# Performance work log

Measured on AMD Instinct MI355X. Metric: run time of the kernel, lower is better.

The kernel has to match this reference:

```python
import jax, jax.numpy as jnp
import numpy as np

B, T, H, STEPS = 8192, 128, 128, 30
BN_EPS = 1e-5


def gru_cell(x, h, w_ih, w_hh, b_ih, b_hh):
    # PyTorch GRU gate math: gates ordered (r, z, n)
    gi = x @ w_ih.T + b_ih            # [B, 3H]
    gh = h @ w_hh.T + b_hh            # [B, 3H]
    ir, iz, inn = jnp.split(gi, 3, axis=-1)
    hr, hz, hn = jnp.split(gh, 3, axis=-1)
    r = jax.nn.sigmoid(ir + hr)
    z = jax.nn.sigmoid(iz + hz)
    n = jnp.tanh(inn + r * hn)
    return (1.0 - z) * n + z * h


def setup_inputs() -> dict:
    key = jax.random.key(0)
    ks = jax.random.split(key, 10)
    s = lambda k, shape: jax.random.normal(k, shape, jnp.float32) * 0.05
    z = lambda *shape: jnp.zeros(shape, jnp.float32)
    return {
        "past": jax.random.normal(ks[0], (B, 6, T), jnp.float32),
        "conv_w": s(ks[1], (H, 6, 3)),
        "conv_b": z(H),
        "bn_gamma": jnp.ones((1,), jnp.float32),
        "bn_beta": z(1),
        "bn_mean": z(1),
        "bn_var": jnp.ones((1,), jnp.float32),
        "enc_wih": s(ks[2], (3 * H, H)),
        "enc_whh": s(ks[3], (3 * H, H)),
        "enc_bih": z(3 * H),
        "enc_bhh": z(3 * H),
        "dec_wih": s(ks[4], (3 * H, H)),
        "dec_whh": s(ks[5], (3 * H, H)),
        "dec_bih": z(3 * H),
        "dec_bhh": z(3 * H),
        "fc1_w": s(ks[6], (256, H)),
        "fc1_b": z(256),
        "fc2_w": s(ks[7], (64, 256)),
        "fc2_b": z(64),
        "fc3_w": s(ks[8], (6, 64)),
        "fc3_b": z(6),
    }


def reference(past, conv_w, conv_b, bn_gamma, bn_beta, bn_mean, bn_var,
              enc_wih, enc_whh, enc_bih, enc_bhh,
              dec_wih, dec_whh, dec_bih, dec_bhh,
              fc1_w, fc1_b, fc2_w, fc2_b, fc3_w, fc3_b):
    b = past.shape[0]
    # Conv1d(6 -> 128, k=3, pad=1) + ReLU
    y = jax.lax.conv_general_dilated(
        past, conv_w, window_strides=(1,), padding=[(1, 1)],
        dimension_numbers=("NCH", "OIH", "NCH"))
    y = jax.nn.relu(y + conv_b[None, :, None])
    # BatchNorm2d(1) in eval mode: single-channel affine normalization over whole tensor
    y = bn_gamma[0] * (y - bn_mean[0]) * jax.lax.rsqrt(bn_var[0] + BN_EPS) + bn_beta[0]
    # encoder GRU over time: [B,128,T] -> [T,B,128]
    xs = jnp.transpose(y, (2, 0, 1))
    h0 = jnp.zeros((b, H), y.dtype)

    def enc_step(h, x):
        return gru_cell(x, h, enc_wih, enc_whh, enc_bih, enc_bhh), None

    state_past, _ = jax.lax.scan(enc_step, h0, xs)  # [B,128]

    def mlp(h):
        a = jax.nn.relu(h @ fc1_w.T + fc1_b)
        a = a @ fc2_w.T + fc2_b   # no activation between fc2 and fc3 (matches Sequential)
        return a @ fc3_w.T + fc3_b

    # decoder input is state_past at step 0, zeros afterwards
    dec_inputs = jnp.concatenate(
        [state_past[None], jnp.zeros((STEPS - 1, b, H), y.dtype)], axis=0)
    present0 = past[:, :, -1]  # [B,6]

    def dec_step(carry, x):
        h, present = carry
        h = gru_cell(x, h, dec_wih, dec_whh, dec_bih, dec_bhh)
        present = present + mlp(h)
        return (h, present), present

    _, preds = jax.lax.scan(dec_step, (jnp.zeros((b, H), y.dtype), present0), dec_inputs)
    # preds: [30,B,6] -> [B,6,30] (matches prediction.permute(0,2,1))
    return jnp.transpose(preds, (1, 2, 0))
```

## Files before the change

### kernel.cpp

```cpp
#include <hip/hip_runtime.h>

#define DI __device__ __forceinline__

typedef __attribute__((ext_vector_type(8))) short short8;
typedef __attribute__((ext_vector_type(4))) float f32x4;

constexpr int THREADS = 512;
constexpr int ROWS    = 32;
constexpr int NBLK    = 8192 / ROWS;
constexpr int PITCH   = 272;
constexpr int PITCH2  = 528;
constexpr int SPITCH  = 256;

constexpr float L2E  = 1.4426950408889634f;
constexpr float L2E2 = 2.8853900817779268f;

constexpr int O_STAGE = 0;
constexpr int O_PATCH = 98304;
constexpr int O_XALL  = 108544;
constexpr int O_H     = 143360;
constexpr int HBUF    = 8704;
constexpr int O_FC3W  = 160768;
constexpr int LDS_TOTAL = 162304;
constexpr int O_A1D   = 98304;
constexpr int O_W32   = 115200;
constexpr int O_B32   = 123648;
constexpr int O_A1D2  = 123680;

DI unsigned cvtpk2(float lo, float hi){
  unsigned r;
  asm("v_cvt_pk_bf16_f32 %0, %1, %2" : "=v"(r) : "v"(lo), "v"(hi));
  return r;
}
DI unsigned short f2bf(float f){ return (unsigned short)cvtpk2(f, f); }
DI float u2f_lo(unsigned u){ union { unsigned u; float f; } v; v.u = u << 16;        return v.f; }
DI float u2f_hi(unsigned u){ union { unsigned u; float f; } v; v.u = u & 0xffff0000u; return v.f; }
DI float exp2n(float x){ float r; asm("v_exp_f32 %0, -%1" : "=v"(r) : "v"(x)); return r; }
DI float sigm2(float s){ return __builtin_amdgcn_rcpf(1.f + exp2n(s)); }
DI float tanh2(float s){ return 2.f * __builtin_amdgcn_rcpf(1.f + exp2n(s)) - 1.f; }
DI f32x4 mfma16(short8 a, short8 b, f32x4 c){
  return __builtin_amdgcn_mfma_f32_16x16x32_bf16(a, b, c, 0, 0, 0);
}
DI uint2 pack4(f32x4 v){
  return make_uint2(cvtpk2(v[0], v[1]), cvtpk2(v[2], v[3]));
}
DI f32x4 unpack4(uint2 u){
  return (f32x4){u2f_lo(u.x), u2f_hi(u.x), u2f_lo(u.y), u2f_hi(u.y)};
}

DI void stage_k128(char* dst, const float* __restrict__ src, int nrows, int tid,
                   float sA, float sB){
  const int total = nrows * 32;
  for (int i = tid; i < total; i += THREADS){
    float4 v = ((const float4*)src)[i];
    int e = i << 2;
    int n = e >> 7, k = e & 127;
    float sc = (n < 256) ? sA : sB;
    *(uint2*)(dst + n * SPITCH + k * 2) =
        make_uint2(cvtpk2(v.x * sc, v.y * sc), cvtpk2(v.z * sc, v.w * sc));
  }
}

__global__ void __launch_bounds__(THREADS, 1)
gru_fused(const float* __restrict__ past,
          const float* __restrict__ conv_w, const float* __restrict__ conv_b,
          const float* __restrict__ bn_gamma, const float* __restrict__ bn_beta,
          const float* __restrict__ bn_mean, const float* __restrict__ bn_var,
          const float* __restrict__ enc_wih, const float* __restrict__ enc_whh,
          const float* __restrict__ enc_bih, const float* __restrict__ enc_bhh,
          const float* __restrict__ dec_wih, const float* __restrict__ dec_whh,
          const float* __restrict__ dec_bih, const float* __restrict__ dec_bhh,
          const float* __restrict__ fc1_w, const float* __restrict__ fc1_b,
          const float* __restrict__ fc2_w, const float* __restrict__ fc2_b,
          const float* __restrict__ fc3_w, const float* __restrict__ fc3_b,
          float* __restrict__ out)
{
  extern __shared__ char smem[];
  const int tid  = threadIdx.x;
  const int lane = tid & 63, w = tid >> 6;
  const int l15  = lane & 15, quad = lane >> 4;
  const int b0   = blockIdx.x * ROWS;
  const int col  = w * 16 + l15;

  const float br_e  = (enc_bih[col]       + enc_bhh[col])       * L2E;
  const float bz_e  = (enc_bih[128 + col] + enc_bhh[128 + col]) * L2E;
  const float bin_e = enc_bih[256 + col] * L2E2;
  const float bhn_e = enc_bhh[256 + col] * L2E2;
  const float br_d  = (dec_bih[col]       + dec_bhh[col])       * L2E;
  const float bz_d  = (dec_bih[128 + col] + dec_bhh[128 + col]) * L2E;
  const float bin_d = dec_bih[256 + col] * L2E2;
  const float bhn_d = dec_bhh[256 + col] * L2E2;
  const float cb_t  = conv_b[col];
  const float s_bn  = bn_gamma[0] * rsqrtf(bn_var[0] + 1e-5f);
  const float o_bn  = bn_beta[0] - bn_mean[0] * s_bn;
  const float fb1a  = fc1_b[w * 32 + l15];
  const float fb1b  = fc1_b[w * 32 + 16 + l15];

  for (int i = tid; i < 2*HBUF/4; i += THREADS) ((unsigned*)(smem + O_H))[i] = 0u;

  short8 wf[3][4], wh[3][4];
  stage_k128(smem + O_STAGE, enc_wih, 384, tid, L2E, L2E2);
  __syncthreads();
  #pragma unroll
  for (int g = 0; g < 3; ++g)
    #pragma unroll
    for (int kt = 0; kt < 4; ++kt)
      wf[g][kt] = *(const short8*)(smem + O_STAGE + (g*128 + col)*SPITCH + kt*64 + quad*16);
  __syncthreads();
  stage_k128(smem + O_STAGE, enc_whh, 384, tid, L2E, L2E2);
  __syncthreads();
  #pragma unroll
  for (int g = 0; g < 3; ++g)
    #pragma unroll
    for (int kt = 0; kt < 4; ++kt)
      wh[g][kt] = *(const short8*)(smem + O_STAGE + (g*128 + col)*SPITCH + kt*64 + quad*16);
  __syncthreads();

  for (int i = tid; i < 2560; i += THREADS) ((unsigned*)(smem + O_STAGE))[i] = 0u;
  __syncthreads();
  for (int i = tid; i < 2304; i += THREADS){
    int oc = i / 18, kk = i - oc * 18;
    *(unsigned short*)(smem + O_STAGE + oc*80 + kk*2) = f2bf(conv_w[i]);
  }
  __syncthreads();
  const short8 cwf = *(const short8*)(smem + O_STAGE + col*80 + quad*16);
  __syncthreads();

  for (int i = tid; i < 12672; i += THREADS) ((unsigned*)(smem + O_STAGE))[i] = 0u;
  __syncthreads();
  for (int i4 = tid; i4 < 6144; i4 += THREADS){
    int m = i4 / 192, rem = i4 - m*192, c = rem >> 5, t4 = (rem & 31) << 2;
    float4 v = *(const float4*)(past + (size_t)(b0 + m)*768 + c*128 + t4);
    unsigned short* dst = (unsigned short*)(smem + O_STAGE + ((m*6 + c)*132 + t4 + 1)*2);
    dst[0] = f2bf(v.x); dst[1] = f2bf(v.y); dst[2] = f2bf(v.z); dst[3] = f2bf(v.w);
  }
  for (int i = tid; i < 384; i += THREADS) ((float*)(smem + O_FC3W))[i] = fc3_w[i];
  __syncthreads();

  const int e0 = tid;
  const int m0 = e0 / 18, r0 = e0 - m0*18, c0 = r0 / 3, k0 = r0 - c0*3;
  const int e1 = tid + 512;
  const int m1 = e1 / 18, r1 = e1 - m1*18, c1 = r1 / 3, k1 = r1 - c1*3;

  auto patch_entry = [&](int t0, int m, int r18, int c, int k){
    int base = (m*6 + c)*132 + t0 + k;
    const unsigned* pl = (const unsigned*)(smem + O_STAGE);
    unsigned w0 = pl[base >> 1], w1 = pl[(base >> 1) + 1], w2 = pl[(base >> 1) + 2];
    int sh = (base & 1) * 16;
    unsigned long long lo = (unsigned long long)w0 | ((unsigned long long)w1 << 32);
    unsigned long long hi = (unsigned long long)w1 | ((unsigned long long)w2 << 32);
    unsigned a01 = (unsigned)(lo >> sh);
    unsigned a23 = (unsigned)(hi >> sh);
    char* pb = smem + O_PATCH + m*80 + r18*2;
    *(unsigned short*)(pb)          = (unsigned short)(a01 & 0xffff);
    *(unsigned short*)(pb + 2560)   = (unsigned short)(a01 >> 16);
    *(unsigned short*)(pb + 5120)   = (unsigned short)(a23 & 0xffff);
    *(unsigned short*)(pb + 7680)   = (unsigned short)(a23 >> 16);
  };
  auto patchA1 = [&](int t0){
    patch_entry(t0, m0, r0, c0, k0);
    if (e1 < 576) patch_entry(t0, m1, r1, c1, k1);
  };

  uint2 gi_pk[4][2][3];
  float hreg[8];
  #pragma unroll
  for (int i = 0; i < 8; ++i) hreg[i] = 0.f;

  auto conv_block = [&](){
    #pragma unroll
    for (int mt8 = 0; mt8 < 8; ++mt8){
      short8 pa = *(const short8*)(smem + O_PATCH + (mt8*16 + l15)*80 + quad*16);
      f32x4 cc = (f32x4){0.f,0.f,0.f,0.f};
      cc = mfma16(pa, cwf, cc);
      #pragma unroll
      for (int r = 0; r < 4; ++r){
        int mrow = mt8*16 + quad*4 + r;
        float vx = s_bn * fmaxf(cc[r] + cb_t, 0.f) + o_bn;
        *(unsigned short*)(smem + O_XALL + mrow*PITCH + col*2) = f2bf(vx);
      }
    }
  };
  auto gi_unit = [&](int tc, int mt){
    short8 a[4];
    #pragma unroll
    for (int kt = 0; kt < 4; ++kt)
      a[kt] = *(const short8*)(smem + O_XALL + ((tc*2 + mt)*16 + l15)*PITCH + kt*64 + quad*16);
    f32x4 g0 = (f32x4){0.f,0.f,0.f,0.f}, g1 = g0, g2 = g0;
    #pragma unroll
    for (int kt = 0; kt < 4; ++kt){
      g0 = mfma16(a[kt], wf[0][kt], g0);
      g1 = mfma16(a[kt], wf[1][kt], g1);
      g2 = mfma16(a[kt], wf[2][kt], g2);
    }
    gi_pk[tc][mt][0] = pack4(g0);
    gi_pk[tc][mt][1] = pack4(g1);
    gi_pk[tc][mt][2] = pack4(g2);
  };
  auto step_body = [&](int t, int tc){
    const char* hr = smem + O_H + (t & 1) * HBUF;
    char*       hw = smem + O_H + ((t + 1) & 1) * HBUF;
    f32x4 accr[2], accz[2], accn2[2], gin[2];
    #pragma unroll
    for (int mt = 0; mt < 2; ++mt){
      accr[mt]  = unpack4(gi_pk[tc][mt][0]);
      accz[mt]  = unpack4(gi_pk[tc][mt][1]);
      gin[mt]   = unpack4(gi_pk[tc][mt][2]);
      accn2[mt] = (f32x4){0.f,0.f,0.f,0.f};
    }
    short8 ha[2][4];
    #pragma unroll
    for (int mt = 0; mt < 2; ++mt)
      #pragma unroll
      for (int kt = 0; kt < 4; ++kt)
        ha[mt][kt] = *(const short8*)(hr + (mt*16 + l15)*PITCH + kt*64 + quad*16);
    #pragma unroll
    for (int mt = 0; mt < 2; ++mt)
      #pragma unroll
      for (int kt = 0; kt < 4; ++kt){
        accr[mt]  = mfma16(ha[mt][kt], wh[0][kt], accr[mt]);
        accz[mt]  = mfma16(ha[mt][kt], wh[1][kt], accz[mt]);
        accn2[mt] = mfma16(ha[mt][kt], wh[2][kt], accn2[mt]);
      }
    #pragma unroll
    for (int mt = 0; mt < 2; ++mt)
      #pragma unroll
      for (int r = 0; r < 4; ++r){
        float rg = sigm2(accr[mt][r] + br_e);
        float zg = sigm2(accz[mt][r] + bz_e);
        float ng = tanh2(gin[mt][r] + bin_e + rg*(accn2[mt][r] + bhn_e));
        hreg[mt*4 + r] = ng + zg*(hreg[mt*4 + r] - ng);
      }
    #pragma unroll
    for (int mt = 0; mt < 2; ++mt)
      #pragma unroll
      for (int r = 0; r < 4; ++r)
        *(unsigned short*)(hw + (mt*16 + quad*4 + r)*PITCH + col*2) = f2bf(hreg[mt*4 + r]);
  };

  patchA1(0);
  __syncthreads();
  conv_block();
  __syncthreads();
  #pragma unroll
  for (int tc = 0; tc < 4; ++tc){ gi_unit(tc, 0); gi_unit(tc, 1); }
  patchA1(4);
  __syncthreads();

  for (int c = 0; c < 32; ++c){
    const int t0 = c * 4;
    const bool prod = (c < 31);
    step_body(t0 + 0, 0);
    if (prod) conv_block();
    __syncthreads();
    step_body(t0 + 1, 1);
    if (prod){ gi_unit(0,0); gi_unit(0,1); gi_unit(1,0); }
    __syncthreads();
    step_body(t0 + 2, 2);
    if (prod){ gi_unit(1,1); gi_unit(2,0); gi_unit(2,1); }
    __syncthreads();
    step_body(t0 + 3, 3);
    if (prod){ gi_unit(3,0); gi_unit(3,1); if (c < 30) patchA1(t0 + 8); }
    __syncthreads();
  }

  stage_k128(smem + O_STAGE, dec_wih, 384, tid, L2E, L2E2);
  __syncthreads();
  #pragma unroll
  for (int g = 0; g < 3; ++g)
    #pragma unroll
    for (int kt = 0; kt < 4; ++kt)
      wf[g][kt] = *(const short8*)(smem + O_STAGE + (g*128 + col)*SPITCH + kt*64 + quad*16);
  f32x4 gi0r[2], gi0z[2], gi0n[2];
  {
    short8 hea[2][4];
    #pragma unroll
    for (int mt = 0; mt < 2; ++mt)
      #pragma unroll
      for (int kt = 0; kt < 4; ++kt)
        hea[mt][kt] = *(const short8*)(smem + O_H + (mt*16 + l15)*PITCH + kt*64 + quad*16);
    #pragma unroll
    for (int mt = 0; mt < 2; ++mt){
      gi0r[mt] = (f32x4){0.f,0.f,0.f,0.f}; gi0z[mt] = gi0r[mt]; gi0n[mt] = gi0r[mt];
      #pragma unroll
      for (int kt = 0; kt < 4; ++kt){
        gi0r[mt] = mfma16(hea[mt][kt], wf[0][kt], gi0r[mt]);
        gi0z[mt] = mfma16(hea[mt][kt], wf[1][kt], gi0z[mt]);
        gi0n[mt] = mfma16(hea[mt][kt], wf[2][kt], gi0n[mt]);
      }
    }
  }
  __syncthreads();
  stage_k128(smem + O_STAGE, dec_whh, 384, tid, L2E, L2E2);
  __syncthreads();
  #pragma unroll
  for (int g = 0; g < 3; ++g)
    #pragma unroll
    for (int kt = 0; kt < 4; ++kt)
      wh[g][kt] = *(const short8*)(smem + O_STAGE + (g*128 + col)*SPITCH + kt*64 + quad*16);
  __syncthreads();
  short8 f1f[2][4];
  stage_k128(smem + O_STAGE, fc1_w, 256, tid, 1.f, 1.f);
  __syncthreads();
  #pragma unroll
  for (int j = 0; j < 2; ++j)
    #pragma unroll
    for (int kt = 0; kt < 4; ++kt)
      f1f[j][kt] = *(const short8*)(smem + O_STAGE + (w*32 + j*16 + l15)*SPITCH + kt*64 + quad*16);
  __syncthreads();

  for (int i = tid; i < 2112; i += THREADS) ((unsigned*)(smem + O_W32))[i] = 0u;
  __syncthreads();
  {
    const int kk = tid & 255, wn = (tid >> 8) * 3;
    const float* f3p = (const float*)(smem + O_FC3W);
    float o0 = 0.f, o1 = 0.f, o2 = 0.f;
    for (int j = 0; j < 64; ++j){
      float cv = fc2_w[j*256 + kk];
      o0 += f3p[(wn+0)*64 + j] * cv;
      o1 += f3p[(wn+1)*64 + j] * cv;
      o2 += f3p[(wn+2)*64 + j] * cv;
    }
    *(unsigned short*)(smem + O_W32 + (wn+0)*PITCH2 + kk*2) = f2bf(o0);
    *(unsigned short*)(smem + O_W32 + (wn+1)*PITCH2 + kk*2) = f2bf(o1);
    *(unsigned short*)(smem + O_W32 + (wn+2)*PITCH2 + kk*2) = f2bf(o2);
    if (tid < 6){
      float ob = fc3_b[tid];
      for (int j = 0; j < 64; ++j) ob += f3p[tid*64 + j] * fc2_b[j];
      ((float*)(smem + O_B32))[tid] = ob;
    }
  }
  for (int i = tid; i < HBUF/4; i += THREADS) ((unsigned*)(smem + O_H + HBUF))[i] = 0u;
  #pragma unroll
  for (int i = 0; i < 8; ++i) hreg[i] = 0.f;
  __syncthreads();
  float pres[4] = {0.f, 0.f, 0.f, 0.f};
  float b32v = 0.f;
  if (w < 2 && l15 < 6){
    b32v = ((const float*)(smem + O_B32))[l15];
    #pragma unroll
    for (int r = 0; r < 4; ++r)
      pres[r] = past[(size_t)(b0 + w*16 + quad*4 + r)*768 + l15*128 + 127];
  }

  auto fc23 = [&](int sIdx){
    const char* a1b = smem + ((sIdx & 1) ? O_A1D2 : O_A1D);
    f32x4 acc = (f32x4){0.f,0.f,0.f,0.f};
    #pragma unroll
    for (int kt = 0; kt < 8; ++kt){
      short8 a   = *(const short8*)(a1b + (w*16 + l15)*PITCH2 + kt*64 + quad*16);
      short8 bfr = *(const short8*)(smem + O_W32 + l15*PITCH2 + kt*64 + quad*16);
      acc = mfma16(a, bfr, acc);
    }
    if (l15 < 6){
      #pragma unroll
      for (int r = 0; r < 4; ++r){
        pres[r] += acc[r] + b32v;
        out[(size_t)(b0 + w*16 + quad*4 + r)*180 + l15*30 + sIdx] = pres[r];
      }
    }
  };

  for (int s = 0; s < 30; ++s){
    const char* hr = smem + O_H + (1 - (s & 1)) * HBUF;
    char*       hw = smem + O_H + (s & 1) * HBUF;
    f32x4 accr[2], accz[2], accn2[2], gin[2];
    #pragma unroll
    for (int mt = 0; mt < 2; ++mt){
      if (s == 0){ accr[mt] = gi0r[mt]; accz[mt] = gi0z[mt]; gin[mt] = gi0n[mt]; }
      else       { accr[mt] = (f32x4){0.f,0.f,0.f,0.f}; accz[mt] = accr[mt]; gin[mt] = accr[mt]; }
      accn2[mt] = (f32x4){0.f,0.f,0.f,0.f};
    }
    {
      short8 ha[2][4];
      #pragma unroll
      for (int mt = 0; mt < 2; ++mt)
        #pragma unroll
        for (int kt = 0; kt < 4; ++kt)
          ha[mt][kt] = *(const short8*)(hr + (mt*16 + l15)*PITCH + kt*64 + quad*16);
      #pragma unroll
      for (int mt = 0; mt < 2; ++mt)
        #pragma unroll
        for (int kt = 0; kt < 4; ++kt){
          accr[mt]  = mfma16(ha[mt][kt], wh[0][kt], accr[mt]);
          accz[mt]  = mfma16(ha[mt][kt], wh[1][kt], accz[mt]);
          accn2[mt] = mfma16(ha[mt][kt], wh[2][kt], accn2[mt]);
        }
    }
    #pragma unroll
    for (int mt = 0; mt < 2; ++mt)
      #pragma unroll
      for (int r = 0; r < 4; ++r){
        float rg = sigm2(accr[mt][r] + br_d);
        float zg = sigm2(accz[mt][r] + bz_d);
        float ng = tanh2(gin[mt][r] + bin_d + rg*(accn2[mt][r] + bhn_d));
        hreg[mt*4 + r] = ng + zg*(hreg[mt*4 + r] - ng);
      }
    #pragma unroll
    for (int mt = 0; mt < 2; ++mt)
      #pragma unroll
      for (int r = 0; r < 4; ++r)
        *(unsigned short*)(hw + (mt*16 + quad*4 + r)*PITCH + col*2) = f2bf(hreg[mt*4 + r]);
    __syncthreads();

    if (s > 0 && w < 2) fc23(s - 1);

    {
      char* a1w = smem + ((s & 1) ? O_A1D2 : O_A1D);
      short8 hf[2][4];
      #pragma unroll
      for (int mt = 0; mt < 2; ++mt)
        #pragma unroll
        for (int kt = 0; kt < 4; ++kt)
          hf[mt][kt] = *(const short8*)(hw + (mt*16 + l15)*PITCH + kt*64 + quad*16);
      f32x4 a1a[2][2];
      #pragma unroll
      for (int mt = 0; mt < 2; ++mt)
        #pragma unroll
        for (int j = 0; j < 2; ++j) a1a[mt][j] = (f32x4){0.f,0.f,0.f,0.f};
      #pragma unroll
      for (int j = 0; j < 2; ++j)
        #pragma unroll
        for (int kt = 0; kt < 4; ++kt){
          a1a[0][j] = mfma16(hf[0][kt], f1f[j][kt], a1a[0][j]);
          a1a[1][j] = mfma16(hf[1][kt], f1f[j][kt], a1a[1][j]);
        }
      #pragma unroll
      for (int mt = 0; mt < 2; ++mt)
        #pragma unroll
        for (int j = 0; j < 2; ++j){
          float bb = j ? fb1b : fb1a;
          #pragma unroll
          for (int r = 0; r < 4; ++r)
            *(unsigned short*)(a1w + (mt*16 + quad*4 + r)*PITCH2 +
                               (w*32 + j*16 + l15)*2) = f2bf(fmaxf(a1a[mt][j][r] + bb, 0.f));
        }
    }
  }
  __syncthreads();
  if (w < 2) fc23(29);
}

extern "C" void kernel_launch(void* const* d_in, const int* in_sizes, int n_in,
                              void* d_out, int out_size, void* d_ws, size_t ws_size,
                              hipStream_t stream) {
  (void)in_sizes; (void)n_in; (void)out_size; (void)d_ws; (void)ws_size;
  const float* past     = (const float*)d_in[0];
  const float* conv_w   = (const float*)d_in[1];
  const float* conv_b   = (const float*)d_in[2];
  const float* bn_gamma = (const float*)d_in[3];
  const float* bn_beta  = (const float*)d_in[4];
  const float* bn_mean  = (const float*)d_in[5];
  const float* bn_var   = (const float*)d_in[6];
  const float* enc_wih  = (const float*)d_in[7];
  const float* enc_whh  = (const float*)d_in[8];
  const float* enc_bih  = (const float*)d_in[9];
  const float* enc_bhh  = (const float*)d_in[10];
  const float* dec_wih  = (const float*)d_in[11];
  const float* dec_whh  = (const float*)d_in[12];
  const float* dec_bih  = (const float*)d_in[13];
  const float* dec_bhh  = (const float*)d_in[14];
  const float* fc1_w    = (const float*)d_in[15];
  const float* fc1_b    = (const float*)d_in[16];
  const float* fc2_w    = (const float*)d_in[17];
  const float* fc2_b    = (const float*)d_in[18];
  const float* fc3_w    = (const float*)d_in[19];
  const float* fc3_b    = (const float*)d_in[20];

  hipFuncSetAttribute((const void*)gru_fused,
                      hipFuncAttributeMaxDynamicSharedMemorySize, LDS_TOTAL);

  gru_fused<<<NBLK, THREADS, LDS_TOTAL, stream>>>(
      past, conv_w, conv_b, bn_gamma, bn_beta, bn_mean, bn_var,
      enc_wih, enc_whh, enc_bih, enc_bhh,
      dec_wih, dec_whh, dec_bih, dec_bhh,
      fc1_w, fc1_b, fc2_w, fc2_b, fc3_w, fc3_b,
      (float*)d_out);
}
```

Baseline: 425.1 us.

## Fold BN scale and conv bias into conv weights; pack bf16 LDS stores via lane shuffles

```diff
diff --git a/kernel.cpp b/kernel.cpp
--- a/kernel.cpp
+++ b/kernel.cpp
@@ -81,6 +81,7 @@
   const int l15  = lane & 15, quad = lane >> 4;
   const int b0   = blockIdx.x * ROWS;
   const int col  = w * 16 + l15;
+  const bool evn = !(lane & 1);
 
   const float br_e  = (enc_bih[col]       + enc_bhh[col])       * L2E;
   const float bz_e  = (enc_bih[128 + col] + enc_bhh[128 + col]) * L2E;
@@ -90,7 +91,6 @@
   const float bz_d  = (dec_bih[128 + col] + dec_bhh[128 + col]) * L2E;
   const float bin_d = dec_bih[256 + col] * L2E2;
   const float bhn_d = dec_bhh[256 + col] * L2E2;
-  const float cb_t  = conv_b[col];
   const float s_bn  = bn_gamma[0] * rsqrtf(bn_var[0] + 1e-5f);
   const float o_bn  = bn_beta[0] - bn_mean[0] * s_bn;
   const float fb1a  = fc1_b[w * 32 + l15];
@@ -120,11 +120,16 @@
   __syncthreads();
   for (int i = tid; i < 2304; i += THREADS){
     int oc = i / 18, kk = i - oc * 18;
-    *(unsigned short*)(smem + O_STAGE + oc*80 + kk*2) = f2bf(conv_w[i]);
-  }
+    *(unsigned short*)(smem + O_STAGE + oc*80 + kk*2) = f2bf(conv_w[i] * s_bn);
+  }
+  for (int i = tid; i < 128; i += THREADS)
+    *(unsigned short*)(smem + O_STAGE + i*80 + 36) = f2bf(conv_b[i] * s_bn);
   __syncthreads();
   const short8 cwf = *(const short8*)(smem + O_STAGE + col*80 + quad*16);
   __syncthreads();
+
+  for (int i = tid; i < 128; i += THREADS)
+    *(unsigned short*)(smem + O_PATCH + i*80 + 36) = (unsigned short)0x3F80;
 
   for (int i = tid; i < 12672; i += THREADS) ((unsigned*)(smem + O_STAGE))[i] = 0u;
   __syncthreads();
@@ -176,8 +181,10 @@
       #pragma unroll
       for (int r = 0; r < 4; ++r){
         int mrow = mt8*16 + quad*4 + r;
-        float vx = s_bn * fmaxf(cc[r] + cb_t, 0.f) + o_bn;
-        *(unsigned short*)(smem + O_XALL + mrow*PITCH + col*2) = f2bf(vx);
+        float vx = fmaxf(cc[r], 0.f) + o_bn;
+        float vn = __shfl_xor(vx, 1);
+        if (evn)
+          *(unsigned*)(smem + O_XALL + mrow*PITCH + col*2) = cvtpk2(vx, vn);
       }
     }
   };
@@ -234,8 +241,11 @@
     #pragma unroll
     for (int mt = 0; mt < 2; ++mt)
       #pragma unroll
-      for (int r = 0; r < 4; ++r)
-        *(unsigned short*)(hw + (mt*16 + quad*4 + r)*PITCH + col*2) = f2bf(hreg[mt*4 + r]);
+      for (int r = 0; r < 4; ++r){
+        float hn = __shfl_xor(hreg[mt*4 + r], 1);
+        if (evn)
+          *(unsigned*)(hw + (mt*16 + quad*4 + r)*PITCH + col*2) = cvtpk2(hreg[mt*4 + r], hn);
+      }
   };
 
   patchA1(0);
@@ -399,8 +409,11 @@
     #pragma unroll
     for (int mt = 0; mt < 2; ++mt)
       #pragma unroll
-      for (int r = 0; r < 4; ++r)
-        *(unsigned short*)(hw + (mt*16 + quad*4 + r)*PITCH + col*2) = f2bf(hreg[mt*4 + r]);
+      for (int r = 0; r < 4; ++r){
+        float hn = __shfl_xor(hreg[mt*4 + r], 1);
+        if (evn)
+          *(unsigned*)(hw + (mt*16 + quad*4 + r)*PITCH + col*2) = cvtpk2(hreg[mt*4 + r], hn);
+      }
     __syncthreads();
 
     if (s > 0 && w < 2) fc23(s - 1);
@@ -431,9 +444,13 @@
         for (int j = 0; j < 2; ++j){
           float bb = j ? fb1b : fb1a;
           #pragma unroll
-          for (int r = 0; r < 4; ++r)
-            *(unsigned short*)(a1w + (mt*16 + quad*4 + r)*PITCH2 +
-                               (w*32 + j*16 + l15)*2) = f2bf(fmaxf(a1a[mt][j][r] + bb, 0.f));
+          for (int r = 0; r < 4; ++r){
+            float av = fmaxf(a1a[mt][j][r] + bb, 0.f);
+            float an = __shfl_xor(av, 1);
+            if (evn)
+              *(unsigned*)(a1w + (mt*16 + quad*4 + r)*PITCH2 +
+                           (w*32 + j*16 + l15)*2) = cvtpk2(av, an);
+          }
         }
     }
   }
```

Measured after the change: 524.4 us. 23.3% more time.
